# Kernel tuning notes

Hardware: AMD Instinct MI355X
Metric: run time of the kernel (lower is better)

## Reference

```python
import jax, jax.numpy as jnp
import numpy as np

D_MODEL = 1024
NUM_HEADS = 16
D_K = D_MODEL // NUM_HEADS


def setup_inputs() -> dict:
    key = jax.random.key(0)
    ks = jax.random.split(key, 7)
    B, S = 2, 2048
    scale = 1.0 / np.sqrt(D_MODEL)
    return {
        "Q": jax.random.normal(ks[0], (B, S, D_MODEL), dtype=jnp.float32),
        "K": jax.random.normal(ks[1], (B, S, D_MODEL), dtype=jnp.float32),
        "V": jax.random.normal(ks[2], (B, S, D_MODEL), dtype=jnp.float32),
        "W_q": jax.random.normal(ks[3], (D_MODEL, D_MODEL), dtype=jnp.float32) * scale,
        "W_k": jax.random.normal(ks[4], (D_MODEL, D_MODEL), dtype=jnp.float32) * scale,
        "W_v": jax.random.normal(ks[5], (D_MODEL, D_MODEL), dtype=jnp.float32) * scale,
        "W_o": jax.random.normal(ks[6], (D_MODEL, D_MODEL), dtype=jnp.float32) * scale,
    }


def _split_heads(x):
    B, S, _ = x.shape
    return x.reshape(B, S, NUM_HEADS, D_K).transpose(0, 2, 1, 3)  # [B,H,S,Dk]


def reference(Q, K, V, W_q, W_k, W_v, W_o):
    # nn.Linear(bias=False): x @ W.T
    q = _split_heads(Q @ W_q.T)
    k = _split_heads(K @ W_k.T)
    v = _split_heads(V @ W_v.T)
    scores = jnp.einsum("bhqd,bhkd->bhqk", q, k) / jnp.sqrt(jnp.float32(D_K))
    probs = jax.nn.softmax(scores, axis=-1)
    out = jnp.einsum("bhqk,bhkd->bhqd", probs, v)  # [B,H,S,Dk]
    B, H, S, Dk = out.shape
    out = out.transpose(0, 2, 1, 3).reshape(B, S, H * Dk)
    return out @ W_o.T
```

## Files before the change

kernel.cpp:

```cpp
#include <hip/hip_runtime.h>
#include <cstdint>

#define D_MODEL 1024
#define NH 16
#define DK 64
#define SEQ 2048
#define BATCH 2
#define M_TOT (BATCH * SEQ)

typedef __bf16 bf16x8          __attribute__((ext_vector_type(8)));
typedef unsigned short u16x8   __attribute__((ext_vector_type(8)));
typedef float  f32x4           __attribute__((ext_vector_type(4)));

union pun8 { u16x8 u; bf16x8 b; };

__device__ __forceinline__ f32x4 mfma16(bf16x8 a, bf16x8 b, f32x4 c) {
    return __builtin_amdgcn_mfma_f32_16x16x32_bf16(a, b, c, 0, 0, 0);
}

__device__ __forceinline__ unsigned short f2bf(float f) {
    union { float f; uint32_t u; } v; v.f = f;
    uint32_t u = v.u;
    return (unsigned short)((u + 0x7FFFu + ((u >> 16) & 1u)) >> 16);
}

__device__ __forceinline__ unsigned short f2bf_trunc(float f) {
    union { float f; uint32_t u; } v; v.f = f;
    return (unsigned short)(v.u >> 16);
}

__device__ __forceinline__ void gl_lds16(const unsigned short* g, unsigned short* l) {
    __builtin_amdgcn_global_load_lds(
        (const __attribute__((address_space(1))) void*)g,
        (__attribute__((address_space(3))) void*)l, 16, 0, 0);
}

#define C_EXP2 0.1803368801111204f

__global__ __launch_bounds__(256) void convert_all_kernel(
    const float* __restrict__ Q,  const float* __restrict__ K,
    const float* __restrict__ V,  const float* __restrict__ Wq,
    const float* __restrict__ Wk, const float* __restrict__ Wv,
    const float* __restrict__ Wo,
    unsigned short* __restrict__ Qb,  unsigned short* __restrict__ Kb,
    unsigned short* __restrict__ Vb,  unsigned short* __restrict__ Wqb,
    unsigned short* __restrict__ Wkb, unsigned short* __restrict__ Wvb,
    unsigned short* __restrict__ Wob)
{
    int bid = blockIdx.x;
    const float* src; unsigned short* dst; int base;
    if (bid < 3 * 2048) {
        int r = bid >> 11;
        src  = (r == 0) ? Q  : (r == 1) ? K  : V;
        dst  = (r == 0) ? Qb : (r == 1) ? Kb : Vb;
        base = (bid & 2047) * 2048;
    } else {
        int u = bid - 3 * 2048;
        int r = u >> 9;
        src  = (r == 0) ? Wq  : (r == 1) ? Wk  : (r == 2) ? Wv  : Wo;
        dst  = (r == 0) ? Wqb : (r == 1) ? Wkb : (r == 2) ? Wvb : Wob;
        base = (u & 511) * 2048;
    }
    int i = base + threadIdx.x * 8;
    float4 a = *(const float4*)(src + i);
    float4 b = *(const float4*)(src + i + 4);
    u16x8 o;
    o[0] = f2bf(a.x); o[1] = f2bf(a.y); o[2] = f2bf(a.z); o[3] = f2bf(a.w);
    o[4] = f2bf(b.x); o[5] = f2bf(b.y); o[6] = f2bf(b.z); o[7] = f2bf(b.w);
    *(u16x8*)(dst + i) = o;
}

__global__ __launch_bounds__(256) void qkv_proj_kernel(
    const unsigned short* __restrict__ Q,
    const unsigned short* __restrict__ K,
    const unsigned short* __restrict__ V,
    const unsigned short* __restrict__ Wq,
    const unsigned short* __restrict__ Wk,
    const unsigned short* __restrict__ Wv,
    unsigned short* __restrict__ qb,
    unsigned short* __restrict__ kb,
    unsigned short* __restrict__ vtb)
{
    const int z = blockIdx.z;
    const unsigned short* A  = (z == 0) ? Q  : (z == 1) ? K  : V;
    const unsigned short* Bt = (z == 0) ? Wq : (z == 1) ? Wk : Wv;

    const int m0 = blockIdx.y * 128;
    const int n0 = blockIdx.x * 128;

    __shared__ __align__(16) unsigned short smem[128 * 136];
    unsigned short* As = smem;
    unsigned short* Bs = smem + 128 * 64;
    unsigned short* Cs = smem;

    const int t    = threadIdx.x;
    const int lane = t & 63;
    const int w    = t >> 6;
    const int l15  = lane & 15;
    const int quad = lane >> 4;
    const int wm   = (w >> 1) * 64;
    const int wn   = (w & 1) * 64;

    f32x4 acc[4][4] = {};

    for (int k0 = 0; k0 < D_MODEL; k0 += 64) {
        __syncthreads();
        #pragma unroll
        for (int i = 0; i < 4; i++) {
            int u   = t + i * 256;
            int row = u >> 3;
            int kc  = (u & 7) * 8;
            gl_lds16(&A [(m0 + row) * D_MODEL + k0 + kc], &As[(i * 256 + w * 64) * 8]);
            gl_lds16(&Bt[(n0 + row) * D_MODEL + k0 + kc], &Bs[(i * 256 + w * 64) * 8]);
        }
        __syncthreads();

        #pragma unroll
        for (int kk = 0; kk < 2; kk++) {
            bf16x8 a[4], b[4];
            #pragma unroll
            for (int mi = 0; mi < 4; mi++)
                a[mi] = *(const bf16x8*)(&As[(wm + mi * 16 + l15) * 64 + kk * 32 + quad * 8]);
            #pragma unroll
            for (int ni = 0; ni < 4; ni++)
                b[ni] = *(const bf16x8*)(&Bs[(wn + ni * 16 + l15) * 64 + kk * 32 + quad * 8]);

            #pragma unroll
            for (int mi = 0; mi < 4; mi++)
                #pragma unroll
                for (int ni = 0; ni < 4; ni++)
                    acc[mi][ni] = mfma16(a[mi], b[ni], acc[mi][ni]);
        }
    }

    const float oscale = (z == 0) ? C_EXP2 : 1.0f;
    __syncthreads();
    #pragma unroll
    for (int mi = 0; mi < 4; mi++) {
        #pragma unroll
        for (int ni = 0; ni < 4; ni++) {
            #pragma unroll
            for (int r = 0; r < 4; r++) {
                int rloc = wm + mi * 16 + quad * 4 + r;
                int cloc = wn + ni * 16 + l15;
                int rr = (z == 2) ? cloc : rloc;
                int cc = (z == 2) ? rloc : cloc;
                Cs[rr * 136 + cc] = f2bf(acc[mi][ni][r] * oscale);
            }
        }
    }
    __syncthreads();
    #pragma unroll
    for (int i = 0; i < 8; i++) {
        int u    = t + i * 256;
        int rrow = u >> 4;
        int cc8  = (u & 15) * 8;
        u16x8 val = *(const u16x8*)(&Cs[rrow * 136 + cc8]);
        unsigned short* dst;
        if (z < 2) {
            int m = m0 + rrow, n = n0 + cc8;
            int bi = m >> 11, s = m & (SEQ - 1);
            int hh = n >> 6,  d = n & (DK - 1);
            dst = ((z == 0) ? qb : kb) + (((size_t)(bi * NH + hh) * SEQ + s) * DK + d);
        } else {
            int dglob = n0 + rrow;
            int bi = m0 >> 11, s = (m0 & (SEQ - 1)) + cc8;
            int hh = dglob >> 6, d = dglob & (DK - 1);
            dst = vtb + (((size_t)(bi * NH + hh) * DK + d) * SEQ + s);
        }
        *(u16x8*)dst = val;
    }
}

__global__ __launch_bounds__(256) void attn_kernel(
    const unsigned short* __restrict__ qb,
    const unsigned short* __restrict__ kb,
    const unsigned short* __restrict__ vtb,
    unsigned short* __restrict__ ctx)
{
    const int h  = blockIdx.x;
    const int qt = blockIdx.y;
    const int b  = blockIdx.z;

    const int t    = threadIdx.x;
    const int lane = t & 63;
    const int w    = t >> 6;
    const int l15  = lane & 15;
    const int quad = lane >> 4;

    const unsigned short* qh = qb  + ((b * NH + h) * SEQ) * DK;
    const unsigned short* kh = kb  + ((b * NH + h) * SEQ) * DK;
    const unsigned short* vh = vtb + ((b * NH + h) * DK) * SEQ;

    __shared__ __align__(16) unsigned short p_lds[4][32][72];
    __shared__ __align__(16) unsigned short Ks[128 * 72];
    __shared__ __align__(16) unsigned short Vs[64 * 136];

    const int qrow0 = qt * 128 + w * 32;
    bf16x8 qa[2][2];
    #pragma unroll
    for (int m = 0; m < 2; m++)
        #pragma unroll
        for (int kk = 0; kk < 2; kk++)
            qa[m][kk] = *(const bf16x8*)(&qh[(qrow0 + m * 16 + l15) * DK + kk * 32 + quad * 8]);

    pun8 ones_p;
    #pragma unroll
    for (int i = 0; i < 8; i++) ones_p.u[i] = 0x3F80;
    const bf16x8 ones = ones_p.b;

    f32x4 o[2][4] = {};
    f32x4 lacc[2] = {};

    for (int kt = 0; kt < SEQ / 128; kt++) {
        __syncthreads();
        #pragma unroll
        for (int i = 0; i < 4; i++) {
            int u   = t + i * 256;
            int row = u >> 3;
            int c8  = (u & 7) * 8;
            *(u16x8*)(&Ks[row * 72 + c8]) =
                *(const u16x8*)(&kh[(kt * 128 + row) * DK + c8]);
        }
        #pragma unroll
        for (int i = 0; i < 4; i++) {
            int u   = t + i * 256;
            int row = u >> 4;
            int c8  = (u & 15) * 8;
            *(u16x8*)(&Vs[row * 136 + c8]) =
                *(const u16x8*)(&vh[row * SEQ + kt * 128 + c8]);
        }
        __syncthreads();

        #pragma unroll
        for (int hh = 0; hh < 2; hh++) {
            bf16x8 kf[4][2], vf[4][2];
            #pragma unroll
            for (int nb = 0; nb < 4; nb++) {
                const int krow = hh * 64 + nb * 16 + l15;
                kf[nb][0] = *(const bf16x8*)(&Ks[krow * 72 + quad * 8]);
                kf[nb][1] = *(const bf16x8*)(&Ks[krow * 72 + 32 + quad * 8]);
            }
            #pragma unroll
            for (int db = 0; db < 4; db++) {
                vf[db][0] = *(const bf16x8*)(&Vs[(db * 16 + l15) * 136 + hh * 64 + quad * 8]);
                vf[db][1] = *(const bf16x8*)(&Vs[(db * 16 + l15) * 136 + hh * 64 + 32 + quad * 8]);
            }

            f32x4 sacc[2][4] = {};
            #pragma unroll
            for (int m = 0; m < 2; m++)
                #pragma unroll
                for (int nb = 0; nb < 4; nb++) {
                    sacc[m][nb] = mfma16(qa[m][0], kf[nb][0], sacc[m][nb]);
                    sacc[m][nb] = mfma16(qa[m][1], kf[nb][1], sacc[m][nb]);
                }

            #pragma unroll
            for (int m = 0; m < 2; m++)
                #pragma unroll
                for (int nb = 0; nb < 4; nb++)
                    #pragma unroll
                    for (int r = 0; r < 4; r++) {
                        float p = exp2f(sacc[m][nb][r]);
                        p_lds[w][m * 16 + quad * 4 + r][nb * 16 + l15] = f2bf_trunc(p);
                    }

            asm volatile("" ::: "memory");

            bf16x8 pa[2][2];
            #pragma unroll
            for (int m = 0; m < 2; m++)
                #pragma unroll
                for (int kk = 0; kk < 2; kk++)
                    pa[m][kk] = *(const bf16x8*)(&p_lds[w][m * 16 + l15][kk * 32 + quad * 8]);

            asm volatile("" ::: "memory");

            #pragma unroll
            for (int db = 0; db < 4; db++)
                #pragma unroll
                for (int m = 0; m < 2; m++) {
                    o[m][db] = mfma16(pa[m][0], vf[db][0], o[m][db]);
                    o[m][db] = mfma16(pa[m][1], vf[db][1], o[m][db]);
                }

            #pragma unroll
            for (int m = 0; m < 2; m++) {
                lacc[m] = mfma16(pa[m][0], ones, lacc[m]);
                lacc[m] = mfma16(pa[m][1], ones, lacc[m]);
            }
        }
    }

    #pragma unroll
    for (int m = 0; m < 2; m++) {
        const int srow_base = b * SEQ + qt * 128 + w * 32 + m * 16 + quad * 4;
        #pragma unroll
        for (int db = 0; db < 4; db++)
            #pragma unroll
            for (int r = 0; r < 4; r++) {
                float val = o[m][db][r] / lacc[m][r];
                ctx[(srow_base + r) * D_MODEL + h * DK + db * 16 + l15] = f2bf(val);
            }
    }
}

__global__ __launch_bounds__(256) void out_proj_kernel(
    const unsigned short* __restrict__ A,
    const unsigned short* __restrict__ Bt,
    float* __restrict__ out)
{
    const int m0 = blockIdx.y * 64;
    const int n0 = blockIdx.x * 128;

    __shared__ __align__(16) unsigned short As[64 * 64];
    __shared__ __align__(16) unsigned short Bs[128 * 64];

    const int t    = threadIdx.x;
    const int lane = t & 63;
    const int w    = t >> 6;
    const int l15  = lane & 15;
    const int quad = lane >> 4;
    const int wn   = w * 32;

    f32x4 acc[4][2] = {};

    for (int k0 = 0; k0 < D_MODEL; k0 += 64) {
        __syncthreads();
        #pragma unroll
        for (int i = 0; i < 2; i++) {
            int u   = t + i * 256;
            int row = u >> 3;
            int kc  = (u & 7) * 8;
            gl_lds16(&A[(m0 + row) * D_MODEL + k0 + kc], &As[(i * 256 + w * 64) * 8]);
        }
        #pragma unroll
        for (int i = 0; i < 4; i++) {
            int u   = t + i * 256;
            int row = u >> 3;
            int kc  = (u & 7) * 8;
            gl_lds16(&Bt[(n0 + row) * D_MODEL + k0 + kc], &Bs[(i * 256 + w * 64) * 8]);
        }
        __syncthreads();

        #pragma unroll
        for (int kk = 0; kk < 2; kk++) {
            bf16x8 a[4], bfr[2];
            #pragma unroll
            for (int mi = 0; mi < 4; mi++)
                a[mi] = *(const bf16x8*)(&As[(mi * 16 + l15) * 64 + kk * 32 + quad * 8]);
            #pragma unroll
            for (int ni = 0; ni < 2; ni++)
                bfr[ni] = *(const bf16x8*)(&Bs[(wn + ni * 16 + l15) * 64 + kk * 32 + quad * 8]);

            #pragma unroll
            for (int mi = 0; mi < 4; mi++)
                #pragma unroll
                for (int ni = 0; ni < 2; ni++)
                    acc[mi][ni] = mfma16(a[mi], bfr[ni], acc[mi][ni]);
        }
    }

    #pragma unroll
    for (int mi = 0; mi < 4; mi++) {
        #pragma unroll
        for (int ni = 0; ni < 2; ni++) {
            #pragma unroll
            for (int r = 0; r < 4; r++) {
                int m = m0 + mi * 16 + quad * 4 + r;
                int n = n0 + wn + ni * 16 + l15;
                out[m * D_MODEL + n] = acc[mi][ni][r];
            }
        }
    }
}

extern "C" void kernel_launch(void* const* d_in, const int* in_sizes, int n_in,
                              void* d_out, int out_size, void* d_ws, size_t ws_size,
                              hipStream_t stream) {
    const float* Q  = (const float*)d_in[0];
    const float* K  = (const float*)d_in[1];
    const float* V  = (const float*)d_in[2];
    const float* Wq = (const float*)d_in[3];
    const float* Wk = (const float*)d_in[4];
    const float* Wv = (const float*)d_in[5];
    const float* Wo = (const float*)d_in[6];

    const size_t NQ = (size_t)M_TOT * D_MODEL;
    const size_t NW = (size_t)D_MODEL * D_MODEL;

    unsigned short* Qb  = (unsigned short*)d_ws;
    unsigned short* Kb  = Qb  + NQ;
    unsigned short* Vb  = Kb  + NQ;
    unsigned short* Wqb = Vb  + NQ;
    unsigned short* Wkb = Wqb + NW;
    unsigned short* Wvb = Wkb + NW;
    unsigned short* Wob = Wvb + NW;
    unsigned short* qb  = Wob + NW;
    unsigned short* kbf = qb  + NQ;
    unsigned short* vtb = kbf + NQ;
    unsigned short* ctx = vtb + NQ;
    float* out = (float*)d_out;

    convert_all_kernel<<<3 * 2048 + 4 * 512, 256, 0, stream>>>(
        Q, K, V, Wq, Wk, Wv, Wo, Qb, Kb, Vb, Wqb, Wkb, Wvb, Wob);

    dim3 g1(D_MODEL / 128, M_TOT / 128, 3);
    qkv_proj_kernel<<<g1, 256, 0, stream>>>(Qb, Kb, Vb, Wqb, Wkb, Wvb, qb, kbf, vtb);

    dim3 g2(NH, SEQ / 128, BATCH);
    attn_kernel<<<g2, 256, 0, stream>>>(qb, kbf, vtb, ctx);

    dim3 g3(D_MODEL / 128, M_TOT / 64, 1);
    out_proj_kernel<<<g3, 256, 0, stream>>>(ctx, Wob, out);
}
```

Baseline: 231.3 us.

## Software-pipeline PV MFMA one step behind QK in attention kernel

Restructures the attention inner loop so the P·V and row-sum MFMAs of the previous half-tile run while the current half-tile's exp/softmax and P LDS round-trip are done. P and V fragments are carried across iterations in registers, with an epilogue that drains the last step. It also adds s_setprio around the MFMA blocks and a min-2-blocks launch bound. The intent is to overlap matrix-core work with the exp and LDS work. In exchange it raises register pressure, and the occupancy bound could cause spills.

```diff
diff --git a/kernel.cpp b/kernel.cpp
--- a/kernel.cpp
+++ b/kernel.cpp
@@ -172,7 +172,7 @@
     }
 }
 
-__global__ __launch_bounds__(256) void attn_kernel(
+__global__ __launch_bounds__(256, 2) void attn_kernel(
     const unsigned short* __restrict__ qb,
     const unsigned short* __restrict__ kb,
     const unsigned short* __restrict__ vtb,
@@ -212,6 +212,9 @@
     f32x4 o[2][4] = {};
     f32x4 lacc[2] = {};
 
+    bf16x8 pa_p[2][2] = {};
+    bf16x8 vf_p[4][2] = {};
+
     for (int kt = 0; kt < SEQ / 128; kt++) {
         __syncthreads();
         #pragma unroll
@@ -234,20 +237,16 @@
 
         #pragma unroll
         for (int hh = 0; hh < 2; hh++) {
-            bf16x8 kf[4][2], vf[4][2];
+            bf16x8 kf[4][2];
             #pragma unroll
             for (int nb = 0; nb < 4; nb++) {
                 const int krow = hh * 64 + nb * 16 + l15;
                 kf[nb][0] = *(const bf16x8*)(&Ks[krow * 72 + quad * 8]);
                 kf[nb][1] = *(const bf16x8*)(&Ks[krow * 72 + 32 + quad * 8]);
             }
-            #pragma unroll
-            for (int db = 0; db < 4; db++) {
-                vf[db][0] = *(const bf16x8*)(&Vs[(db * 16 + l15) * 136 + hh * 64 + quad * 8]);
-                vf[db][1] = *(const bf16x8*)(&Vs[(db * 16 + l15) * 136 + hh * 64 + 32 + quad * 8]);
-            }
 
             f32x4 sacc[2][4] = {};
+            __builtin_amdgcn_s_setprio(1);
             #pragma unroll
             for (int m = 0; m < 2; m++)
                 #pragma unroll
@@ -255,6 +254,29 @@
                     sacc[m][nb] = mfma16(qa[m][0], kf[nb][0], sacc[m][nb]);
                     sacc[m][nb] = mfma16(qa[m][1], kf[nb][1], sacc[m][nb]);
                 }
+            __builtin_amdgcn_s_setprio(0);
+
+            bf16x8 vf_c[4][2];
+            #pragma unroll
+            for (int db = 0; db < 4; db++) {
+                vf_c[db][0] = *(const bf16x8*)(&Vs[(db * 16 + l15) * 136 + hh * 64 + quad * 8]);
+                vf_c[db][1] = *(const bf16x8*)(&Vs[(db * 16 + l15) * 136 + hh * 64 + 32 + quad * 8]);
+            }
+
+            __builtin_amdgcn_s_setprio(1);
+            #pragma unroll
+            for (int db = 0; db < 4; db++)
+                #pragma unroll
+                for (int m = 0; m < 2; m++) {
+                    o[m][db] = mfma16(pa_p[m][0], vf_p[db][0], o[m][db]);
+                    o[m][db] = mfma16(pa_p[m][1], vf_p[db][1], o[m][db]);
+                }
+            #pragma unroll
+            for (int m = 0; m < 2; m++) {
+                lacc[m] = mfma16(pa_p[m][0], ones, lacc[m]);
+                lacc[m] = mfma16(pa_p[m][1], ones, lacc[m]);
+            }
+            __builtin_amdgcn_s_setprio(0);
 
             #pragma unroll
             for (int m = 0; m < 2; m++)
@@ -268,30 +290,36 @@
 
             asm volatile("" ::: "memory");
 
-            bf16x8 pa[2][2];
             #pragma unroll
             for (int m = 0; m < 2; m++)
                 #pragma unroll
                 for (int kk = 0; kk < 2; kk++)
-                    pa[m][kk] = *(const bf16x8*)(&p_lds[w][m * 16 + l15][kk * 32 + quad * 8]);
+                    pa_p[m][kk] = *(const bf16x8*)(&p_lds[w][m * 16 + l15][kk * 32 + quad * 8]);
 
             asm volatile("" ::: "memory");
 
             #pragma unroll
-            for (int db = 0; db < 4; db++)
-                #pragma unroll
-                for (int m = 0; m < 2; m++) {
-                    o[m][db] = mfma16(pa[m][0], vf[db][0], o[m][db]);
-                    o[m][db] = mfma16(pa[m][1], vf[db][1], o[m][db]);
-                }
-
-            #pragma unroll
-            for (int m = 0; m < 2; m++) {
-                lacc[m] = mfma16(pa[m][0], ones, lacc[m]);
-                lacc[m] = mfma16(pa[m][1], ones, lacc[m]);
-            }
-        }
-    }
+            for (int db = 0; db < 4; db++) {
+                vf_p[db][0] = vf_c[db][0];
+                vf_p[db][1] = vf_c[db][1];
+            }
+        }
+    }
+
+    __builtin_amdgcn_s_setprio(1);
+    #pragma unroll
+    for (int db = 0; db < 4; db++)
+        #pragma unroll
+        for (int m = 0; m < 2; m++) {
+            o[m][db] = mfma16(pa_p[m][0], vf_p[db][0], o[m][db]);
+            o[m][db] = mfma16(pa_p[m][1], vf_p[db][1], o[m][db]);
+        }
+    #pragma unroll
+    for (int m = 0; m < 2; m++) {
+        lacc[m] = mfma16(pa_p[m][0], ones, lacc[m]);
+        lacc[m] = mfma16(pa_p[m][1], ones, lacc[m]);
+    }
+    __builtin_amdgcn_s_setprio(0);
 
     #pragma unroll
     for (int m = 0; m < 2; m++) {
```

New measurement: 230.8 us. About the same (-0.2%).
